# Performance work log

Hardware: AMD Instinct MI355X
Metric: run time of the kernel (lower is better)

## Reference

```python
import jax, jax.numpy as jnp
import numpy as np

EPS = 1e-5
K = 20  # knn3(K=20) is hardcoded in the torch module


def _bn_lrelu(x, g, b, axes):
    # training-mode BatchNorm (batch statistics) + LeakyReLU(0.2)
    m = jnp.mean(x, axis=axes, keepdims=True)
    v = jnp.var(x, axis=axes, keepdims=True)
    y = (x - m) * jax.lax.rsqrt(v + EPS) * g + b
    return jax.nn.leaky_relu(y, 0.2)


def _pool(pts, feat, num_pool):
    # pts: [B,N,3] coords, feat: [B,N,C]. KNN of first num_pool points vs all
    # points, gather neighbor features, max over the K neighbors.
    sub = pts[:, :num_pool]                                   # [B,M,3]
    d2 = (jnp.sum(sub * sub, -1)[:, :, None]
          + jnp.sum(pts * pts, -1)[:, None, :]
          - 2.0 * jnp.einsum('bmd,bnd->bmn', sub, pts))       # [B,M,N]
    idx = jax.lax.top_k(-d2, K)[1]                            # [B,M,K]
    gathered = jax.vmap(lambda f, i: f[i])(feat, idx)         # [B,M,K,C]
    return sub, jnp.max(gathered, axis=2)                     # [B,M,C]


def setup_inputs() -> dict:
    key = jax.random.key(0)
    ks = jax.random.split(key, 16)
    f32 = jnp.float32
    def n(k, shape, s):
        return jax.random.normal(k, shape, dtype=f32) * s
    emb = 1024
    return {
        'x': jax.random.normal(ks[0], (16, 3, 4096), dtype=f32),
        'w1': n(ks[1], (64, 3), 0.5), 'g1': jnp.ones(64, f32), 'b1': jnp.zeros(64, f32),
        'w2': n(ks[2], (64, 64), 0.12), 'g2': jnp.ones(64, f32), 'b2': jnp.zeros(64, f32),
        'w3': n(ks[3], (128, 64), 0.12), 'g3': jnp.ones(128, f32), 'b3': jnp.zeros(128, f32),
        'w4': n(ks[4], (256, 128), 0.09), 'g4': jnp.ones(256, f32), 'b4': jnp.zeros(256, f32),
        'w5': n(ks[5], (emb, 512), 0.045), 'g5': jnp.ones(emb, f32), 'b5': jnp.zeros(emb, f32),
        'l1w': n(ks[6], (512, 2 * emb), 0.022), 'g6': jnp.ones(512, f32), 'b6': jnp.zeros(512, f32),
        'l2w': n(ks[7], (256, 512), 0.045), 'l2b': jnp.zeros(256, f32),
        'g7': jnp.ones(256, f32), 'b7': jnp.zeros(256, f32),
        'l3w': n(ks[8], (40, 256), 0.06), 'l3b': jnp.zeros(40, f32),
    }


def reference(x, w1, g1, b1, w2, g2, b2, w3, g3, b3, w4, g4, b4,
              w5, g5, b5, l1w, g6, b6, l2w, l2b, g7, b7, l3w, l3b):
    B, _, N = x.shape
    pts = jnp.transpose(x, (0, 2, 1))                 # [B,N,3]
    f = _bn_lrelu(pts @ w1.T, g1, b1, (0, 1))         # conv1 -> [B,N,64]
    p, f = _pool(pts, f, N // 4)
    _, x1 = _pool(p, f, N // 64)                      # [B,N/64,64]
    f = _bn_lrelu(f @ w2.T, g2, b2, (0, 1))           # conv2
    p, f = _pool(p, f, N // 16)
    _, x2 = _pool(p, f, N // 64)                      # [B,N/64,64]
    f = _bn_lrelu(f @ w3.T, g3, b3, (0, 1))           # conv3
    p, f = _pool(p, f, N // 32)
    _, x3 = _pool(p, f, N // 64)                      # [B,N/64,128]
    f = _bn_lrelu(f @ w4.T, g4, b4, (0, 1))           # conv4
    p, f = _pool(p, f, N // 64)                       # [B,N/64,256]
    h = jnp.concatenate([x1, x2, x3, f], axis=-1)     # [B,N/64,512]
    h = _bn_lrelu(h @ w5.T, g5, b5, (0, 1))           # conv5 -> [B,N/64,emb]
    h = jnp.concatenate([jnp.max(h, axis=1), jnp.mean(h, axis=1)], axis=-1)
    h = _bn_lrelu(h @ l1w.T, g6, b6, (0,))            # linear1 (no bias)
    h = _bn_lrelu(h @ l2w.T + l2b, g7, b7, (0,))      # linear2; dropout = eval identity
    return h @ l3w.T + l3b                            # [B,40]
```

## Files before the change

kernel.cpp:

```cpp
#include <hip/hip_runtime.h>

#define BN_EPS 1e-5f
#define KNN 20

static inline int ceildiv(int a, int b) { return (a + b - 1) / b; }

__device__ __forceinline__ unsigned long long shflxor64(unsigned long long v, int m, int w) {
    int lo = __shfl_xor((int)(unsigned)(v & 0xffffffffull), m, w);
    int hi = __shfl_xor((int)(unsigned)(v >> 32), m, w);
    return ((unsigned long long)(unsigned)hi << 32) | (unsigned)lo;
}

__global__ void moments3_kernel(const float* __restrict__ x, int N,
                                float* __restrict__ part ,
                                float4* __restrict__ pk ) {
    int b = blockIdx.x;
    int chunk = blockIdx.y;
    int t = threadIdx.x;
    int n0 = chunk * (N >> 2);
    int n1 = n0 + (N >> 2);
    const float* xb = x + (size_t)b * 3 * N;
    float m[9] = {0, 0, 0, 0, 0, 0, 0, 0, 0};
    for (int n = n0 + t; n < n1; n += 256) {
        float px = xb[n], py = xb[N + n], pz = xb[2 * N + n];
        float nr = px * px + py * py + pz * pz;
        pk[(size_t)b * N + n] = make_float4(px, py, pz, nr);
        m[0] += px; m[1] += py; m[2] += pz;
        m[3] += px * px; m[4] += py * py; m[5] += pz * pz;
        m[6] += px * py; m[7] += px * pz; m[8] += py * pz;
    }
#pragma unroll
    for (int o = 32; o; o >>= 1)
#pragma unroll
        for (int i = 0; i < 9; ++i) m[i] += __shfl_down(m[i], o);
    __shared__ float red[4][9];
    if ((t & 63) == 0)
#pragma unroll
        for (int i = 0; i < 9; ++i) red[t >> 6][i] = m[i];
    __syncthreads();
    if (t == 0) {
#pragma unroll
        for (int i = 0; i < 9; ++i)
            part[(b * 4 + chunk) * 9 + i] = red[0][i] + red[1][i] + red[2][i] + red[3][i];
    }
}

__global__ void knn_all_kernel(const float4* __restrict__ pk, int Nstride,
                               int* __restrict__ iA, int* __restrict__ iB,
                               int* __restrict__ iC, int* __restrict__ iD,
                               int* __restrict__ iE, int* __restrict__ iF) {
    int b = blockIdx.y;
    int bx = blockIdx.x;
    int M, N; int* out; int qbase;
    if (bx < 128)      { M = 1024; N = 4096; out = iA; qbase = bx * 8; }
    else if (bx < 136) { M = 64;   N = 1024; out = iB; qbase = (bx - 128) * 8; }
    else if (bx < 168) { M = 256;  N = 1024; out = iC; qbase = (bx - 136) * 8; }
    else if (bx < 176) { M = 64;   N = 256;  out = iD; qbase = (bx - 168) * 8; }
    else if (bx < 192) { M = 128;  N = 256;  out = iE; qbase = (bx - 176) * 8; }
    else               { M = 64;   N = 128;  out = iF; qbase = (bx - 192) * 8; }
    int wave = threadIdx.x >> 6;
    int lane = threadIdx.x & 63;
    int sl = lane & 31;
    int half = lane >> 5;
    int q = qbase + wave * 2 + half;
    const float4* pb = pk + (size_t)b * Nstride;
    float4 qp = pb[q];

    auto dist = [&](int j) -> float {
        float4 c = pb[j];
        return qp.w + c.w - 2.f * (qp.x * c.x + qp.y * c.y + qp.z * c.z);
    };

    int up_addr = ((sl == 0) ? lane : (lane - 1)) << 2;
    int wd_addr = (19 + (half << 5)) << 2;
    int segbyte = half << 7;

    unsigned long long lk;
    {
        float d2 = dist(sl);
        unsigned u = __float_as_uint(d2);
        unsigned ok = (u & 0x80000000u) ? ~u : (u | 0x80000000u);
        lk = ((unsigned long long)ok << 32) | (unsigned)sl;
    }
#pragma unroll
    for (int size = 2; size <= 32; size <<= 1) {
#pragma unroll
        for (int stride = size >> 1; stride >= 1; stride >>= 1) {
            unsigned long long p = shflxor64(lk, stride, 32);
            bool ascend = (sl & size) == 0;
            bool low = (sl & stride) == 0;
            bool keepMin = (ascend == low);
            bool pLess = p < lk;
            lk = (keepMin == pLess) ? p : lk;
        }
    }
    unsigned okey = (unsigned)(lk >> 32);
    unsigned du = (okey & 0x80000000u) ? (okey ^ 0x80000000u) : ~okey;
    float ld = __uint_as_float(du);
    int li = (int)(unsigned)(lk & 0xffffffffull);
    float wd = __uint_as_float(__builtin_amdgcn_ds_bpermute(wd_addr, (int)__float_as_uint(ld)));

    auto insert2 = [&](float dc, int jb, unsigned long long msk) {
        unsigned mlo = (unsigned)msk, mhi = (unsigned)(msk >> 32);
        while (mlo | mhi) {
            int slo = __ffs((int)mlo) - 1;
            int shi = __ffs((int)mhi) - 1;
            int srcl = half ? shi : slo;
            int addr = ((srcl & 31) << 2) + segbyte;
            float d = __uint_as_float(__builtin_amdgcn_ds_bpermute(addr, (int)__float_as_uint(dc)));
            if (srcl < 0) d = 3.4e38f;
            int id = jb + (srcl & 31);
            float up_d = __uint_as_float(__builtin_amdgcn_ds_bpermute(up_addr, (int)__float_as_uint(ld)));
            int up_i = __builtin_amdgcn_ds_bpermute(up_addr, li);
            bool c = d < ld;
            bool cp = (sl != 0) && (d < up_d);
            ld = c ? (cp ? up_d : d) : ld;
            li = c ? (cp ? up_i : id) : li;
            mlo &= mlo - 1;
            mhi &= mhi - 1;
        }
    };

    {
        float dc = dist(32 + sl);
        unsigned long long m = __ballot(dc < wd);
        if (m) {
            insert2(dc, 32, m);
            wd = __uint_as_float(__builtin_amdgcn_ds_bpermute(wd_addr, (int)__float_as_uint(ld)));
        }
    }
    for (int j0 = 64; j0 < N; j0 += 64) {
        float dc0 = dist(j0 + sl);
        float dc1 = dist(j0 + 32 + sl);
        unsigned long long m0 = __ballot(dc0 < wd);
        unsigned long long m1 = __ballot(dc1 < wd);
        if (m0 | m1) {
            if (m0) insert2(dc0, j0, m0);
            if (m1) insert2(dc1, j0 + 32, m1);
            wd = __uint_as_float(__builtin_amdgcn_ds_bpermute(wd_addr, (int)__float_as_uint(ld)));
        }
    }
    if (sl < KNN) out[((size_t)b * M + q) * KNN + sl] = li;
}

__global__ void pool1_kernel(const float4* __restrict__ pk, int N, const int* __restrict__ idxA,
                             const float* __restrict__ w1, const float* __restrict__ mom,
                             const float* __restrict__ g, const float* __restrict__ bb,
                             float Rinv, int nparts, float* __restrict__ out, int M) {
    __shared__ float S[9];
    __shared__ float sca[64], shb[64];
    int c = threadIdx.x;
    int tid = threadIdx.y * 64 + c;
    if (tid < 9) {
        float s = 0.f;
        for (int bi = 0; bi < nparts; ++bi) s += mom[bi * 9 + tid];
        S[tid] = s;
    }
    __syncthreads();
    if (tid < 64) {
        float wx = w1[tid * 3], wy = w1[tid * 3 + 1], wz = w1[tid * 3 + 2];
        float mean = (wx * S[0] + wy * S[1] + wz * S[2]) * Rinv;
        float e2 = (wx * wx * S[3] + wy * wy * S[4] + wz * wz * S[5] +
                    2.f * (wx * wy * S[6] + wx * wz * S[7] + wy * wz * S[8])) * Rinv;
        float var = e2 - mean * mean;
        float a = g[tid] * rsqrtf(var + BN_EPS);
        sca[tid] = a;
        shb[tid] = bb[tid] - mean * a;
    }
    __syncthreads();
    int m = blockIdx.x * 4 + threadIdx.y;
    int b = blockIdx.y;
    const float4* pb = pk + (size_t)b * N;
    const int* ip = idxA + ((size_t)b * M + m) * KNN;
    float wx = w1[c * 3], wy = w1[c * 3 + 1], wz = w1[c * 3 + 2];
    float mx = -3.4e38f, mn = 3.4e38f;
#pragma unroll
    for (int k = 0; k < KNN; ++k) {
        float4 p = pb[ip[k]];
        float d = wx * p.x + wy * p.y + wz * p.z;
        mx = fmaxf(mx, d); mn = fminf(mn, d);
    }
    float a = sca[c];
    float v = a * (a >= 0.f ? mx : mn) + shb[c];
    out[((size_t)b * M + m) * 64 + c] = v >= 0.f ? v : 0.2f * v;
}

__global__ void pool_bn_kernel(const float* __restrict__ f, const int* __restrict__ idx,
                               float* __restrict__ out, int M, int Nf, int C,
                               int out_stride, int out_off, const float* __restrict__ scsh) {
    int c = threadIdx.x;
    int m = blockIdx.x * blockDim.y + threadIdx.y;
    int b = blockIdx.y;
    const int* ip = idx + ((size_t)b * M + m) * KNN;
    const float* fb = f + (size_t)b * Nf * C;
    float mx = -3.4e38f, mn = 3.4e38f;
#pragma unroll
    for (int k = 0; k < KNN; ++k) {
        int j = ip[k];
        float v = fb[(size_t)j * C + c];
        mx = fmaxf(mx, v);
        mn = fminf(mn, v);
    }
    float a = scsh[c];
    float v = a * (a >= 0.f ? mx : mn) + scsh[C + c];
    v = v >= 0.f ? v : 0.2f * v;
    out[((size_t)b * M + m) * out_stride + out_off + c] = v;
}

template <int BM, bool POOL>
__global__ void gemm_kernel(const float* __restrict__ A, const float* __restrict__ W,
                            float* __restrict__ Cout, int M, int N, int K,
                            float* __restrict__ part , int nbn,
                            const float* __restrict__ pf, const int* __restrict__ pidx,
                            float* __restrict__ pout, int pNf, int pC, int pstride, int poff) {
    constexpr int RM = BM / 16;
    int t = threadIdx.x;
    int nbm = M / BM;
    int bx = blockIdx.x;
    if (POOL && bx >= nbm * nbn) {
        int e = bx - nbm * nbn;
        int rows = 256 / pC;
        int bpb = 64 / rows;
        int b = e / bpb, mi = e % bpb;
        int m = mi * rows + t / pC;
        int c = t % pC;
        const int* ip = pidx + ((size_t)b * 64 + m) * KNN;
        const float* fb = pf + (size_t)b * pNf * pC;
        float mx = -3.4e38f;
#pragma unroll
        for (int k = 0; k < KNN; ++k) mx = fmaxf(mx, fb[(size_t)ip[k] * pC + c]);
        pout[((size_t)b * 64 + m) * pstride + poff + c] = mx;
        return;
    }
    int bm = bx / nbn, bn = bx % nbn;
    __shared__ float As[16][BM + 4], Ws[16][68];
    int tx = t & 15, ty = t >> 4;
    const float* Ab = A + (size_t)bm * BM * K;
    const float* Wb = W + (size_t)bn * 64 * K;
    float acc[RM][4] = {};
    for (int k0 = 0; k0 < K; k0 += 16) {
#pragma unroll
        for (int r = 0; r < RM; ++r) {
            int row = ty + r * 16;
            As[tx][row] = Ab[(size_t)row * K + k0 + tx];
        }
#pragma unroll
        for (int r = 0; r < 4; ++r) {
            int row = ty + r * 16;
            Ws[tx][row] = Wb[(size_t)row * K + k0 + tx];
        }
        __syncthreads();
#pragma unroll
        for (int kk = 0; kk < 16; ++kk) {
            float av[RM];
#pragma unroll
            for (int i = 0; i < RM; ++i) av[i] = As[kk][ty * RM + i];
            float4 w4 = *(const float4*)&Ws[kk][tx * 4];
            float wv[4] = {w4.x, w4.y, w4.z, w4.w};
#pragma unroll
            for (int i = 0; i < RM; ++i)
#pragma unroll
                for (int j = 0; j < 4; ++j) acc[i][j] += av[i] * wv[j];
        }
        __syncthreads();
    }
#pragma unroll
    for (int i = 0; i < RM; ++i) {
        float4 v = make_float4(acc[i][0], acc[i][1], acc[i][2], acc[i][3]);
        *(float4*)&Cout[(size_t)(bm * BM + ty * RM + i) * N + bn * 64 + tx * 4] = v;
    }
    __shared__ float2 sred[16][64];
#pragma unroll
    for (int j = 0; j < 4; ++j) {
        float s = 0.f, q = 0.f;
#pragma unroll
        for (int i = 0; i < RM; ++i) { s += acc[i][j]; q += acc[i][j] * acc[i][j]; }
        sred[ty][tx * 4 + j] = make_float2(s, q);
    }
    __syncthreads();
    if (t < 64) {
        float s = 0.f, q = 0.f;
#pragma unroll
        for (int r = 0; r < 16; ++r) { s += sred[r][t].x; q += sred[r][t].y; }
        part[(size_t)bm * 2 * N + bn * 64 + t] = s;
        part[(size_t)bm * 2 * N + N + bn * 64 + t] = q;
    }
}

__global__ void bn_finalize_kernel(const float* __restrict__ part, int nparts, int C, int R,
                                   const float* __restrict__ g, const float* __restrict__ bb,
                                   float* __restrict__ scsh) {
    int c = blockIdx.x;
    int t = threadIdx.x;
    float s = 0.f, q = 0.f;
    for (int k = t; k < nparts; k += 256) {
        s += part[(size_t)k * 2 * C + c];
        q += part[(size_t)k * 2 * C + C + c];
    }
#pragma unroll
    for (int o = 32; o; o >>= 1) { s += __shfl_down(s, o); q += __shfl_down(q, o); }
    __shared__ float2 red[4];
    if ((t & 63) == 0) red[t >> 6] = make_float2(s, q);
    __syncthreads();
    if (t == 0) {
        s = red[0].x + red[1].x + red[2].x + red[3].x;
        q = red[0].y + red[1].y + red[2].y + red[3].y;
        float mean = s / (float)R;
        float var = q / (float)R - mean * mean;
        float a = g[c] * rsqrtf(var + BN_EPS);
        scsh[c] = a;
        scsh[C + c] = bb[c] - mean * a;
    }
}

__global__ void global_pool_bn_kernel(const float* __restrict__ h,
                                      const float* __restrict__ scsh,
                                      float* __restrict__ out) {
    int c = blockIdx.x * 256 + threadIdx.x;
    int b = blockIdx.y;
    const float* hb = h + (size_t)b * 64 * 1024;
    float a = scsh[c], sh = scsh[1024 + c];
    float mx = -3.4e38f, s = 0.f;
    for (int r = 0; r < 64; ++r) {
        float v = a * hb[r * 1024 + c] + sh;
        v = v >= 0.f ? v : 0.2f * v;
        mx = fmaxf(mx, v); s += v;
    }
    out[b * 2048 + c] = mx;
    out[b * 2048 + 1024 + c] = s * (1.f / 64.f);
}

__global__ void head_gemm_kernel(const float* __restrict__ A, const float* __restrict__ W,
                                 const float* __restrict__ bias, float* __restrict__ out,
                                 int N, int K) {
    int n = blockIdx.x * 64 + threadIdx.x;
    int m = blockIdx.y;
    if (n >= N) return;
    const float4* a4 = (const float4*)(A + (size_t)m * K);
    const float4* w4 = (const float4*)(W + (size_t)n * K);
    int K4 = K >> 2;
    float acc0 = 0.f, acc1 = 0.f, acc2 = 0.f, acc3 = 0.f;
    for (int k = 0; k < K4; ++k) {
        float4 a = a4[k], w = w4[k];
        acc0 = fmaf(a.x, w.x, acc0);
        acc1 = fmaf(a.y, w.y, acc1);
        acc2 = fmaf(a.z, w.z, acc2);
        acc3 = fmaf(a.w, w.w, acc3);
    }
    float r = (acc0 + acc1) + (acc2 + acc3);
    if (bias) r += bias[n];
    out[(size_t)m * N + n] = r;
}

__global__ void head_bn_gemm2(const float* __restrict__ Apre,
                              const float* __restrict__ g, const float* __restrict__ bb,
                              const float* __restrict__ W, const float* __restrict__ bias,
                              float* __restrict__ out) {
    __shared__ float An[512];
    __shared__ float red[4][64];
    int t = threadIdx.x;
    int m = blockIdx.y;
    for (int c = t; c < 512; c += 256) {
        float s = 0.f, q = 0.f, vm = 0.f;
#pragma unroll
        for (int r = 0; r < 16; ++r) {
            float v = Apre[r * 512 + c];
            s += v; q += v * v;
            if (r == m) vm = v;
        }
        float mean = s * (1.f / 16.f);
        float var = q * (1.f / 16.f) - mean * mean;
        float a = g[c] * rsqrtf(var + BN_EPS);
        float v = a * (vm - mean) + bb[c];
        An[c] = v >= 0.f ? v : 0.2f * v;
    }
    __syncthreads();
    int nl = t & 63, kq = t >> 6;
    int n = blockIdx.x * 64 + nl;
    const float* wn = W + (size_t)n * 512 + kq * 128;
    const float* an = An + kq * 128;
    float s = 0.f;
    for (int k = 0; k < 128; k += 4) {
        float4 a4 = *(const float4*)&an[k];
        float4 w4 = *(const float4*)&wn[k];
        s += a4.x * w4.x + a4.y * w4.y + a4.z * w4.z + a4.w * w4.w;
    }
    red[kq][nl] = s;
    __syncthreads();
    if (t < 64) {
        float r = red[0][t] + red[1][t] + red[2][t] + red[3][t];
        out[(size_t)m * 256 + blockIdx.x * 64 + t] = r + bias[blockIdx.x * 64 + t];
    }
}

__global__ void head_bn_gemm3(const float* __restrict__ Apre,
                              const float* __restrict__ g, const float* __restrict__ bb,
                              const float* __restrict__ W, const float* __restrict__ bias,
                              float* __restrict__ out) {
    __shared__ float An[256];
    __shared__ float red[4][64];
    int t = threadIdx.x;
    int m = blockIdx.x;
    {
        int c = t;
        float s = 0.f, q = 0.f, vm = 0.f;
#pragma unroll
        for (int r = 0; r < 16; ++r) {
            float v = Apre[r * 256 + c];
            s += v; q += v * v;
            if (r == m) vm = v;
        }
        float mean = s * (1.f / 16.f);
        float var = q * (1.f / 16.f) - mean * mean;
        float a = g[c] * rsqrtf(var + BN_EPS);
        float v = a * (vm - mean) + bb[c];
        An[c] = v >= 0.f ? v : 0.2f * v;
    }
    __syncthreads();
    int nl = t & 63, kq = t >> 6;
    float s = 0.f;
    if (nl < 40) {
        const float* wn = W + (size_t)nl * 256 + kq * 64;
        const float* an = An + kq * 64;
        for (int k = 0; k < 64; k += 4) {
            float4 a4 = *(const float4*)&an[k];
            float4 w4 = *(const float4*)&wn[k];
            s += a4.x * w4.x + a4.y * w4.y + a4.z * w4.z + a4.w * w4.w;
        }
    }
    red[kq][nl] = s;
    __syncthreads();
    if (t < 40) {
        float r = red[0][t] + red[1][t] + red[2][t] + red[3][t];
        out[(size_t)m * 40 + t] = r + bias[t];
    }
}

extern "C" void kernel_launch(void* const* d_in, const int* in_sizes, int n_in,
                              void* d_out, int out_size, void* d_ws, size_t ws_size,
                              hipStream_t stream) {
    const int B = 16, N = 4096;
    const float* x   = (const float*)d_in[0];
    const float* w1  = (const float*)d_in[1];
    const float* g1  = (const float*)d_in[2];
    const float* b1  = (const float*)d_in[3];
    const float* w2  = (const float*)d_in[4];
    const float* g2  = (const float*)d_in[5];
    const float* b2  = (const float*)d_in[6];
    const float* w3  = (const float*)d_in[7];
    const float* g3  = (const float*)d_in[8];
    const float* b3  = (const float*)d_in[9];
    const float* w4  = (const float*)d_in[10];
    const float* g4  = (const float*)d_in[11];
    const float* b4  = (const float*)d_in[12];
    const float* w5  = (const float*)d_in[13];
    const float* g5  = (const float*)d_in[14];
    const float* b5  = (const float*)d_in[15];
    const float* l1w = (const float*)d_in[16];
    const float* g6  = (const float*)d_in[17];
    const float* b6  = (const float*)d_in[18];
    const float* l2w = (const float*)d_in[19];
    const float* l2b = (const float*)d_in[20];
    const float* g7  = (const float*)d_in[21];
    const float* b7  = (const float*)d_in[22];
    const float* l3w = (const float*)d_in[23];
    const float* l3b = (const float*)d_in[24];
    float* outp = (float*)d_out;

    char* ws = (char*)d_ws;
    size_t off = 0;
    auto alloc = [&](size_t bytes) -> void* {
        void* p = ws + off;
        off += (bytes + 255) & ~(size_t)255;
        return p;
    };
    float* f1p   = (float*)alloc((size_t)B * 1024 * 64 * 4);
    float* f2pre = (float*)alloc((size_t)B * 1024 * 64 * 4);
    float* f2p   = (float*)alloc((size_t)B * 256 * 64 * 4);
    float* f3pre = (float*)alloc((size_t)B * 256 * 128 * 4);
    float* f3p   = (float*)alloc((size_t)B * 128 * 128 * 4);
    float* f4pre = (float*)alloc((size_t)B * 128 * 256 * 4);
    float* hcat  = (float*)alloc((size_t)B * 64 * 512 * 4);
    float* h5pre = (float*)alloc((size_t)B * 64 * 1024 * 4);
    float* hg    = (float*)alloc((size_t)B * 2048 * 4);
    float* h6pre = (float*)alloc((size_t)B * 512 * 4);
    float* h7pre = (float*)alloc((size_t)B * 256 * 4);
    int* idxA = (int*)alloc((size_t)B * 1024 * KNN * 4);
    int* idxB = (int*)alloc((size_t)B * 64 * KNN * 4);
    int* idxC = (int*)alloc((size_t)B * 256 * KNN * 4);
    int* idxD = (int*)alloc((size_t)B * 64 * KNN * 4);
    int* idxE = (int*)alloc((size_t)B * 128 * KNN * 4);
    int* idxF = (int*)alloc((size_t)B * 64 * KNN * 4);
    float* mom   = (float*)alloc((size_t)B * 4 * 9 * 4);
    float4* pkbuf = (float4*)alloc((size_t)B * N * 16);
    float* part2 = (float*)alloc((size_t)512 * 2 * 64 * 4);
    float* part3 = (float*)alloc((size_t)128 * 2 * 128 * 4);
    float* part4 = (float*)alloc((size_t)64 * 2 * 256 * 4);
    float* part5 = (float*)alloc((size_t)32 * 2 * 1024 * 4);
    float* sc2 = (float*)alloc(2 * 64 * 4);
    float* sc3 = (float*)alloc(2 * 128 * 4);
    float* sc4 = (float*)alloc(2 * 256 * 4);
    float* sc5 = (float*)alloc(2 * 1024 * 4);

    moments3_kernel<<<dim3(B, 4), 256, 0, stream>>>(x, N, mom, pkbuf);
    knn_all_kernel<<<dim3(200, B), 256, 0, stream>>>(pkbuf, N, idxA, idxB, idxC, idxD, idxE, idxF);

    pool1_kernel<<<dim3(256, B), dim3(64, 4), 0, stream>>>(pkbuf, N, idxA, w1, mom, g1, b1,
                                                           1.f / (B * N), B * 4, f1p, 1024);

    gemm_kernel<32, true><<<dim3(512 + 256), 256, 0, stream>>>(
        f1p, w2, f2pre, B * 1024, 64, 64, part2, 1,
        f1p, idxB, hcat, 1024, 64, 512, 0);
    bn_finalize_kernel<<<dim3(64), 256, 0, stream>>>(part2, 512, 64, B * 1024, g2, b2, sc2);
    pool_bn_kernel<<<dim3(64, B), dim3(64, 4), 0, stream>>>(f2pre, idxC, f2p, 256, 1024, 64, 64, 0, sc2);

    gemm_kernel<32, true><<<dim3(256 + 256), 256, 0, stream>>>(
        f2p, w3, f3pre, B * 256, 128, 64, part3, 2,
        f2p, idxD, hcat, 256, 64, 512, 64);
    bn_finalize_kernel<<<dim3(128), 256, 0, stream>>>(part3, 128, 128, B * 256, g3, b3, sc3);
    pool_bn_kernel<<<dim3(64, B), dim3(128, 2), 0, stream>>>(f3pre, idxE, f3p, 128, 256, 128, 128, 0, sc3);

    gemm_kernel<32, true><<<dim3(256 + 512), 256, 0, stream>>>(
        f3p, w4, f4pre, B * 128, 256, 128, part4, 4,
        f3p, idxF, hcat, 128, 128, 512, 128);
    bn_finalize_kernel<<<dim3(256), 256, 0, stream>>>(part4, 64, 256, B * 128, g4, b4, sc4);
    pool_bn_kernel<<<dim3(64, B), dim3(256, 1), 0, stream>>>(f4pre, idxF, hcat, 64, 128, 256, 512, 256, sc4);

    gemm_kernel<32, false><<<dim3(512), 256, 0, stream>>>(
        hcat, w5, h5pre, B * 64, 1024, 512, part5, 16,
        nullptr, nullptr, nullptr, 0, 1, 0, 0);
    bn_finalize_kernel<<<dim3(1024), 256, 0, stream>>>(part5, 32, 1024, B * 64, g5, b5, sc5);
    global_pool_bn_kernel<<<dim3(4, B), 256, 0, stream>>>(h5pre, sc5, hg);

    head_gemm_kernel<<<dim3(8, B), 64, 0, stream>>>(hg, l1w, nullptr, h6pre, 512, 2048);
    head_bn_gemm2<<<dim3(4, B), 256, 0, stream>>>(h6pre, g6, b6, l2w, l2b, h7pre);
    head_bn_gemm3<<<dim3(B), 256, 0, stream>>>(h7pre, g7, b7, l3w, l3b, outp);
}
```

Measured before the change: 293.8 us.

## Fuse first pooling into KNN kernel, vectorize GEMM tile loads, widen head GEMM

```diff
diff --git a/kernel.cpp b/kernel.cpp
--- a/kernel.cpp
+++ b/kernel.cpp
@@ -46,20 +46,48 @@
 }
 
 __global__ void knn_all_kernel(const float4* __restrict__ pk, int Nstride,
-                               int* __restrict__ iA, int* __restrict__ iB,
+                               const float* __restrict__ mom, int nparts,
+                               const float* __restrict__ w1,
+                               const float* __restrict__ g1, const float* __restrict__ bb1,
+                               float Rinv, float* __restrict__ f1p,
+                               int* __restrict__ iB,
                                int* __restrict__ iC, int* __restrict__ iD,
                                int* __restrict__ iE, int* __restrict__ iF) {
+    __shared__ float S[9];
+    __shared__ float sca[64], shb[64];
+    __shared__ int nidx[4][2][KNN];
     int b = blockIdx.y;
     int bx = blockIdx.x;
     int M, N; int* out; int qbase;
-    if (bx < 128)      { M = 1024; N = 4096; out = iA; qbase = bx * 8; }
+    if (bx < 128)      { M = 1024; N = 4096; out = nullptr; qbase = bx * 8; }
     else if (bx < 136) { M = 64;   N = 1024; out = iB; qbase = (bx - 128) * 8; }
     else if (bx < 168) { M = 256;  N = 1024; out = iC; qbase = (bx - 136) * 8; }
     else if (bx < 176) { M = 64;   N = 256;  out = iD; qbase = (bx - 168) * 8; }
     else if (bx < 192) { M = 128;  N = 256;  out = iE; qbase = (bx - 176) * 8; }
     else               { M = 64;   N = 128;  out = iF; qbase = (bx - 192) * 8; }
-    int wave = threadIdx.x >> 6;
-    int lane = threadIdx.x & 63;
+    bool taskA = (bx < 128);
+    int t = threadIdx.x;
+    if (taskA) {
+        if (t < 9) {
+            float s = 0.f;
+            for (int i = 0; i < nparts; ++i) s += mom[i * 9 + t];
+            S[t] = s;
+        }
+        __syncthreads();
+        if (t < 64) {
+            float wx = w1[t * 3], wy = w1[t * 3 + 1], wz = w1[t * 3 + 2];
+            float mean = (wx * S[0] + wy * S[1] + wz * S[2]) * Rinv;
+            float e2 = (wx * wx * S[3] + wy * wy * S[4] + wz * wz * S[5] +
+                        2.f * (wx * wy * S[6] + wx * wz * S[7] + wy * wz * S[8])) * Rinv;
+            float var = e2 - mean * mean;
+            float a = g1[t] * rsqrtf(var + BN_EPS);
+            sca[t] = a;
+            shb[t] = bb1[t] - mean * a;
+        }
+        __syncthreads();
+    }
+    int wave = t >> 6;
+    int lane = t & 63;
     int sl = lane & 31;
     int half = lane >> 5;
     int q = qbase + wave * 2 + half;
@@ -140,49 +168,30 @@
             wd = __uint_as_float(__builtin_amdgcn_ds_bpermute(wd_addr, (int)__float_as_uint(ld)));
         }
     }
-    if (sl < KNN) out[((size_t)b * M + q) * KNN + sl] = li;
-}
-
-__global__ void pool1_kernel(const float4* __restrict__ pk, int N, const int* __restrict__ idxA,
-                             const float* __restrict__ w1, const float* __restrict__ mom,
-                             const float* __restrict__ g, const float* __restrict__ bb,
-                             float Rinv, int nparts, float* __restrict__ out, int M) {
-    __shared__ float S[9];
-    __shared__ float sca[64], shb[64];
-    int c = threadIdx.x;
-    int tid = threadIdx.y * 64 + c;
-    if (tid < 9) {
-        float s = 0.f;
-        for (int bi = 0; bi < nparts; ++bi) s += mom[bi * 9 + tid];
-        S[tid] = s;
-    }
-    __syncthreads();
-    if (tid < 64) {
-        float wx = w1[tid * 3], wy = w1[tid * 3 + 1], wz = w1[tid * 3 + 2];
-        float mean = (wx * S[0] + wy * S[1] + wz * S[2]) * Rinv;
-        float e2 = (wx * wx * S[3] + wy * wy * S[4] + wz * wz * S[5] +
-                    2.f * (wx * wy * S[6] + wx * wz * S[7] + wy * wz * S[8])) * Rinv;
-        float var = e2 - mean * mean;
-        float a = g[tid] * rsqrtf(var + BN_EPS);
-        sca[tid] = a;
-        shb[tid] = bb[tid] - mean * a;
-    }
-    __syncthreads();
-    int m = blockIdx.x * 4 + threadIdx.y;
-    int b = blockIdx.y;
-    const float4* pb = pk + (size_t)b * N;
-    const int* ip = idxA + ((size_t)b * M + m) * KNN;
+
+    if (!taskA) {
+        if (sl < KNN) out[((size_t)b * M + q) * KNN + sl] = li;
+        return;
+    }
+    if (sl < KNN) nidx[wave][half][sl] = li;
+    __syncthreads();
+    int c = lane;
     float wx = w1[c * 3], wy = w1[c * 3 + 1], wz = w1[c * 3 + 2];
-    float mx = -3.4e38f, mn = 3.4e38f;
-#pragma unroll
-    for (int k = 0; k < KNN; ++k) {
-        float4 p = pb[ip[k]];
-        float d = wx * p.x + wy * p.y + wz * p.z;
-        mx = fmaxf(mx, d); mn = fminf(mn, d);
-    }
-    float a = sca[c];
-    float v = a * (a >= 0.f ? mx : mn) + shb[c];
-    out[((size_t)b * M + m) * 64 + c] = v >= 0.f ? v : 0.2f * v;
+    float a = sca[c], sh = shb[c];
+#pragma unroll
+    for (int hq = 0; hq < 2; ++hq) {
+        float mx = -3.4e38f, mn = 3.4e38f;
+#pragma unroll
+        for (int k = 0; k < KNN; ++k) {
+            float4 p = pb[nidx[wave][hq][k]];
+            float d = wx * p.x + wy * p.y + wz * p.z;
+            mx = fmaxf(mx, d); mn = fminf(mn, d);
+        }
+        float v = a * (a >= 0.f ? mx : mn) + sh;
+        v = v >= 0.f ? v : 0.2f * v;
+        int qq2 = qbase + wave * 2 + hq;
+        f1p[((size_t)b * 1024 + qq2) * 64 + c] = v;
+    }
 }
 
 __global__ void pool_bn_kernel(const float* __restrict__ f, const int* __restrict__ idx,
@@ -238,16 +247,17 @@
     const float* Ab = A + (size_t)bm * BM * K;
     const float* Wb = W + (size_t)bn * 64 * K;
     float acc[RM][4] = {};
+    int srow = t >> 2, skb = (t & 3) << 2;
     for (int k0 = 0; k0 < K; k0 += 16) {
-#pragma unroll
-        for (int r = 0; r < RM; ++r) {
-            int row = ty + r * 16;
-            As[tx][row] = Ab[(size_t)row * K + k0 + tx];
-        }
-#pragma unroll
-        for (int r = 0; r < 4; ++r) {
-            int row = ty + r * 16;
-            Ws[tx][row] = Wb[(size_t)row * K + k0 + tx];
+        if (t < BM * 4) {
+            float4 av = *(const float4*)&Ab[(size_t)srow * K + k0 + skb];
+            As[skb][srow] = av.x; As[skb + 1][srow] = av.y;
+            As[skb + 2][srow] = av.z; As[skb + 3][srow] = av.w;
+        }
+        {
+            float4 wv = *(const float4*)&Wb[(size_t)srow * K + k0 + skb];
+            Ws[skb][srow] = wv.x; Ws[skb + 1][srow] = wv.y;
+            Ws[skb + 2][srow] = wv.z; Ws[skb + 3][srow] = wv.w;
         }
         __syncthreads();
 #pragma unroll
@@ -330,26 +340,25 @@
     out[b * 2048 + 1024 + c] = s * (1.f / 64.f);
 }
 
-__global__ void head_gemm_kernel(const float* __restrict__ A, const float* __restrict__ W,
-                                 const float* __restrict__ bias, float* __restrict__ out,
-                                 int N, int K) {
-    int n = blockIdx.x * 64 + threadIdx.x;
+__global__ void head_gemm_wide(const float* __restrict__ A, const float* __restrict__ W,
+                               float* __restrict__ out, int N, int K) {
+    __shared__ float red[4][64];
+    int t = threadIdx.x;
     int m = blockIdx.y;
-    if (n >= N) return;
-    const float4* a4 = (const float4*)(A + (size_t)m * K);
-    const float4* w4 = (const float4*)(W + (size_t)n * K);
-    int K4 = K >> 2;
-    float acc0 = 0.f, acc1 = 0.f, acc2 = 0.f, acc3 = 0.f;
-    for (int k = 0; k < K4; ++k) {
+    int nl = t & 63, kq = t >> 6;
+    int n = blockIdx.x * 64 + nl;
+    int Kc = K >> 2;
+    const float4* a4 = (const float4*)(A + (size_t)m * K + kq * Kc);
+    const float4* w4 = (const float4*)(W + (size_t)n * K + kq * Kc);
+    float s = 0.f;
+    for (int k = 0; k < (Kc >> 2); ++k) {
         float4 a = a4[k], w = w4[k];
-        acc0 = fmaf(a.x, w.x, acc0);
-        acc1 = fmaf(a.y, w.y, acc1);
-        acc2 = fmaf(a.z, w.z, acc2);
-        acc3 = fmaf(a.w, w.w, acc3);
-    }
-    float r = (acc0 + acc1) + (acc2 + acc3);
-    if (bias) r += bias[n];
-    out[(size_t)m * N + n] = r;
+        s += a.x * w.x + a.y * w.y + a.z * w.z + a.w * w.w;
+    }
+    red[kq][nl] = s;
+    __syncthreads();
+    if (t < 64)
+        out[(size_t)m * N + blockIdx.x * 64 + t] = red[0][t] + red[1][t] + red[2][t] + red[3][t];
 }
 
 __global__ void head_bn_gemm2(const float* __restrict__ Apre,
@@ -485,7 +494,6 @@
     float* hg    = (float*)alloc((size_t)B * 2048 * 4);
     float* h6pre = (float*)alloc((size_t)B * 512 * 4);
     float* h7pre = (float*)alloc((size_t)B * 256 * 4);
-    int* idxA = (int*)alloc((size_t)B * 1024 * KNN * 4);
     int* idxB = (int*)alloc((size_t)B * 64 * KNN * 4);
     int* idxC = (int*)alloc((size_t)B * 256 * KNN * 4);
     int* idxD = (int*)alloc((size_t)B * 64 * KNN * 4);
@@ -503,10 +511,9 @@
     float* sc5 = (float*)alloc(2 * 1024 * 4);
 
     moments3_kernel<<<dim3(B, 4), 256, 0, stream>>>(x, N, mom, pkbuf);
-    knn_all_kernel<<<dim3(200, B), 256, 0, stream>>>(pkbuf, N, idxA, idxB, idxC, idxD, idxE, idxF);
-
-    pool1_kernel<<<dim3(256, B), dim3(64, 4), 0, stream>>>(pkbuf, N, idxA, w1, mom, g1, b1,
-                                                           1.f / (B * N), B * 4, f1p, 1024);
+    knn_all_kernel<<<dim3(200, B), 256, 0, stream>>>(pkbuf, N, mom, B * 4, w1, g1, b1,
+                                                     1.f / (B * N), f1p,
+                                                     idxB, idxC, idxD, idxE, idxF);
 
     gemm_kernel<32, true><<<dim3(512 + 256), 256, 0, stream>>>(
         f1p, w2, f2pre, B * 1024, 64, 64, part2, 1,
@@ -532,7 +539,7 @@
     bn_finalize_kernel<<<dim3(1024), 256, 0, stream>>>(part5, 32, 1024, B * 64, g5, b5, sc5);
     global_pool_bn_kernel<<<dim3(4, B), 256, 0, stream>>>(h5pre, sc5, hg);
 
-    head_gemm_kernel<<<dim3(8, B), 64, 0, stream>>>(hg, l1w, nullptr, h6pre, 512, 2048);
+    head_gemm_wide<<<dim3(8, B), 256, 0, stream>>>(hg, l1w, h6pre, 512, 2048);
     head_bn_gemm2<<<dim3(4, B), 256, 0, stream>>>(h6pre, g6, b6, l2w, l2b, h7pre);
     head_bn_gemm3<<<dim3(B), 256, 0, stream>>>(h7pre, g7, b7, l3w, l3b, outp);
 }
```

Result: faster. 261.6 us (-10.9%).
